# Kernel tuning notes

Hardware: AMD Instinct MI355X
Metric: run time of the kernel (lower is better)

The kernel has to match this reference:

```python
import jax, jax.numpy as jnp
import numpy as np

N_WAY = 64

def setup_inputs() -> dict:
    key = jax.random.key(0)
    k1, k2, k3, k4 = jax.random.split(key, 4)
    S, Q, F, D = 1024, 16384, 2048, 512
    xs = jax.random.normal(k1, (S, F), dtype=jnp.float32)
    ys = jax.random.randint(k2, (S,), 0, N_WAY, dtype=jnp.int64)
    xq = jax.random.normal(k3, (Q, F), dtype=jnp.float32)
    W = jax.random.normal(k4, (F, D), dtype=jnp.float32) * 0.02
    b = jnp.zeros((D,), dtype=jnp.float32)
    return {"xs": xs, "ys": ys, "xq": xq, "W": W, "b": b}

def reference(xs, ys, xq, W, b):
    # encoder: linear projection [*, F] -> [*, D]
    z_s = xs @ W + b            # [S, D]
    z_q = xq @ W + b            # [Q, D]
    # class prototypes: segment mean over support embeddings -> [N_way, D]
    counts = jax.ops.segment_sum(jnp.ones_like(ys, dtype=z_s.dtype), ys, num_segments=N_WAY)
    proto = jax.ops.segment_sum(z_s, ys, num_segments=N_WAY) / jnp.clip(counts, 1.0)[:, None]
    # pairwise squared euclidean distance (expand + pow + sum), [Q, N_way]
    diff = z_q[:, None, :] - proto[None, :, :]   # [Q, N_way, D]
    dists = jnp.sum(diff * diff, axis=-1)
    return -dists
```

## Files before the change

### kernel.cpp

```cpp
#include <hip/hip_runtime.h>


typedef __attribute__((ext_vector_type(8))) short short8;
typedef __attribute__((ext_vector_type(4))) float floatx4;

#define S_ROWS 1024
#define F_DIM  2048
#define D_DIM  512
#define NWAY   64
#define Q_ROWS 16384

static __device__ __forceinline__ unsigned short f2bf(float f) {
  unsigned int u = __float_as_uint(f);
  u += 0x7FFF + ((u >> 16) & 1);
  return (unsigned short)(u >> 16);
}
static __device__ __forceinline__ float bf2f(unsigned short s) {
  return __uint_as_float(((unsigned int)s) << 16);
}

static __device__ __forceinline__ void load_lds16(const unsigned short* g, unsigned short* l) {
  __builtin_amdgcn_global_load_lds((const __attribute__((address_space(1))) unsigned int*)g,
                                   (__attribute__((address_space(3))) unsigned int*)l,
                                   16, 0, 0);
}

__global__ __launch_bounds__(256) void k0_transpose(const float* __restrict__ W,
                                                    unsigned short* __restrict__ Wt,
                                                    float* __restrict__ outz,
                                                    float* __restrict__ proto_acc) {
  __shared__ unsigned short t[64][65];
  int bx = blockIdx.x;
  int f0 = (bx >> 3) << 6;
  int d0 = (bx & 7) << 6;
  for (int j = 0; j < 16; j++) {
    int lin = j * 256 + threadIdx.x;
    int fl = lin >> 6, dl = lin & 63;
    t[fl][dl] = f2bf(W[(size_t)(f0 + fl) * 512 + d0 + dl]);
  }
  __syncthreads();
  for (int j = 0; j < 16; j++) {
    int lin = j * 256 + threadIdx.x;
    int dl = lin >> 6, fl = lin & 63;
    Wt[(size_t)(d0 + dl) * 2048 + f0 + fl] = t[fl][dl];
  }
  int tid = threadIdx.x;
  float4 zz = {0.f, 0.f, 0.f, 0.f};
#pragma unroll
  for (int p = 0; p < 4; p++)
    *(float4*)&outz[(size_t)bx * 4096 + p * 1024 + tid * 4] = zz;
  if (tid < 128) proto_acc[bx * 128 + tid] = 0.f;
}

__global__ __launch_bounds__(256) void k0_sort(const int* __restrict__ ys,
                                               int* __restrict__ order,
                                               int* __restrict__ starts,
                                               float* __restrict__ counts) {
  __shared__ int cnt[NWAY];
  __shared__ int st[NWAY + 1];
  __shared__ int wp[NWAY];
  int tid = threadIdx.x;
  if (tid < NWAY) cnt[tid] = 0;
  __syncthreads();
  for (int j = tid; j < S_ROWS; j += 256) atomicAdd(&cnt[ys[j]], 1);
  __syncthreads();
  if (tid == 0) {
    int a = 0;
    for (int c = 0; c < NWAY; c++) { st[c] = a; wp[c] = a; a += cnt[c]; }
    st[NWAY] = a;
  }
  __syncthreads();
  for (int j = tid; j < S_ROWS; j += 256) {
    int c = ys[j];
    int p = atomicAdd(&wp[c], 1);
    order[p] = j;
  }
  if (tid < NWAY) counts[tid] = (float)cnt[tid];
  if (tid < NWAY + 1) starts[tid] = st[tid];
}

__global__ __launch_bounds__(256) void k1_csum(const float* __restrict__ xs,
                                               const int* __restrict__ order,
                                               const int* __restrict__ starts,
                                               float* __restrict__ csum) {
  __shared__ int lord[S_ROWS];
  int c = blockIdx.x >> 1;
  int tid = threadIdx.x;
  int s = starts[c], e = starts[c + 1];
  int len = e - s;
  for (int j = tid; j < len; j += 256) lord[j] = order[s + j];
  __syncthreads();
  int f0 = (blockIdx.x & 1) * 1024 + tid * 4;
  float4 a = {0.f, 0.f, 0.f, 0.f};
  for (int i = 0; i < len; i++) {
    float4 v = *(const float4*)&xs[(size_t)lord[i] * F_DIM + f0];
    a.x += v.x; a.y += v.y; a.z += v.z; a.w += v.w;
  }
  *(float4*)&csum[(size_t)c * F_DIM + f0] = a;
}

__global__ __launch_bounds__(256) void k2_proto(const float* __restrict__ W,
                                               const float* __restrict__ csum,
                                               float* __restrict__ proto_acc) {
  __shared__ float cs[256];
  int bx = blockIdx.x;
  int c = bx >> 4;
  int dh = ((bx >> 3) & 1) * 256;
  int fc = (bx & 7) * 256;
  int tid = threadIdx.x;
  cs[tid] = csum[(size_t)c * F_DIM + fc + tid];
  __syncthreads();
  float a0 = 0.f;
#pragma unroll 8
  for (int f = 0; f < 256; f++)
    a0 += cs[f] * W[(size_t)(fc + f) * 512 + dh + tid];
  atomicAdd(&proto_acc[c * 512 + dh + tid], a0);
}

__global__ __launch_bounds__(256) void k2b_finalize(const float* __restrict__ proto_acc,
                                                    const float* __restrict__ b,
                                                    const float* __restrict__ counts,
                                                    unsigned short* __restrict__ proto_bf,
                                                    float* __restrict__ pnorm_part) {
  __shared__ float red[256];
  int n = blockIdx.x, tid = threadIdx.x;
  float cntv = counts[n];
  float inv = 1.f / fmaxf(cntv, 1.f);
  float qsq[2];
#pragma unroll
  for (int h = 0; h < 2; h++) {
    int d = h * 256 + tid;
    float p = (proto_acc[n * 512 + d] + cntv * b[d]) * inv;
    unsigned short hh = f2bf(p);
    proto_bf[(size_t)n * 512 + d] = hh;
    float q = bf2f(hh);
    qsq[h] = q * q;
  }
#pragma unroll
  for (int h = 0; h < 2; h++) {
    __syncthreads();
    red[tid] = qsq[h];
    __syncthreads();
    for (int s = 64; s > 0; s >>= 1) {
      if ((tid & 127) < s) red[tid] += red[tid + s];
      __syncthreads();
    }
    if (tid == 0) pnorm_part[(h * 2 + 0) * 64 + n] = red[0];
    if (tid == 128) pnorm_part[(h * 2 + 1) * 64 + n] = red[128];
  }
}

__global__ __launch_bounds__(256) void k_cvt(const float* __restrict__ xq,
                                             unsigned short* __restrict__ xqb) {
  size_t i = ((size_t)blockIdx.x * 256 + threadIdx.x) * 8;
  float4 v0 = *(const float4*)&xq[i];
  float4 v1 = *(const float4*)&xq[i + 4];
  ushort4 w0, w1;
  w0.x = f2bf(v0.x); w0.y = f2bf(v0.y); w0.z = f2bf(v0.z); w0.w = f2bf(v0.w);
  w1.x = f2bf(v1.x); w1.y = f2bf(v1.y); w1.z = f2bf(v1.z); w1.w = f2bf(v1.w);
  *(ushort4*)&xqb[i] = w0;
  *(ushort4*)&xqb[i + 4] = w1;
}

#define ZS_LD 136
__global__ __launch_bounds__(256) void k3_fused(const unsigned short* __restrict__ xqb,
                                                const unsigned short* __restrict__ Wt,
                                                const float* __restrict__ b,
                                                const unsigned short* __restrict__ proto_bf,
                                                const float* __restrict__ pnorm_part,
                                                float* __restrict__ out) {
  __shared__ __align__(16) char smem[53248];
  unsigned short* lA = (unsigned short*)smem;
  unsigned short* lB = (unsigned short*)(smem + 8192);
  unsigned short* zs = (unsigned short*)smem;
  unsigned short* pb = (unsigned short*)(smem + 34816);
  float* qnf = (float*)(smem + 52224);
  float* pnl = (float*)(smem + 52736);

  int tid = threadIdx.x;
  int bx = blockIdx.x;
  int xcd = bx & 7;
  int g = bx >> 3;
  int m0 = (xcd * 16 + (g & 15)) * 128;
  int n0 = (g >> 4) * 128;
  int slice = g >> 4;

  int wave = tid >> 6, lane = tid & 63;
  int wm = (wave & 1) * 64, wn = (wave >> 1) * 64;
  int lrow = lane & 15, lquad = lane >> 4;

  floatx4 acc[4][4];
#pragma unroll
  for (int i = 0; i < 4; i++)
#pragma unroll
    for (int j = 0; j < 4; j++) acc[i][j] = (floatx4){0.f, 0.f, 0.f, 0.f};

  int c0 = wave * 64 + lane;

  for (int k0 = 0; k0 < F_DIM; k0 += 32) {
#pragma unroll
    for (int i = 0; i < 2; i++) {
      int c = i * 256 + c0;
      int row = c >> 2, k8 = (c & 3) * 8;
      load_lds16(&xqb[(size_t)(m0 + row) * F_DIM + k0 + k8],
                 &lA[(size_t)(i * 256 + wave * 64) * 8]);
      load_lds16(&Wt[(size_t)(n0 + row) * F_DIM + k0 + k8],
                 &lB[(size_t)(i * 256 + wave * 64) * 8]);
    }
    __syncthreads();
    short8 af[4], bfr[4];
#pragma unroll
    for (int i = 0; i < 4; i++) af[i] = *(const short8*)&lA[(wm + i * 16 + lrow) * 32 + lquad * 8];
#pragma unroll
    for (int j = 0; j < 4; j++) bfr[j] = *(const short8*)&lB[(wn + j * 16 + lrow) * 32 + lquad * 8];
#pragma unroll
    for (int i = 0; i < 4; i++)
#pragma unroll
      for (int j = 0; j < 4; j++)
        acc[i][j] = __builtin_amdgcn_mfma_f32_16x16x32_bf16(af[i], bfr[j], acc[i][j], 0, 0, 0);
    __syncthreads();
  }

  if (tid < 128) qnf[tid] = 0.f;
  if (tid < 64) pnl[tid] = pnorm_part[slice * 64 + tid];
  __syncthreads();

#pragma unroll
  for (int i = 0; i < 4; i++) {
    float rn[4] = {0.f, 0.f, 0.f, 0.f};
#pragma unroll
    for (int j = 0; j < 4; j++) {
      int ld = wn + j * 16 + lrow;
      float bb = b[n0 + ld];
#pragma unroll
      for (int r = 0; r < 4; r++) {
        int rl = wm + i * 16 + lquad * 4 + r;
        float v = acc[i][j][r] + bb;
        unsigned short h = f2bf(v);
        zs[rl * ZS_LD + ld] = h;
        float vq = bf2f(h);
        rn[r] += vq * vq;
      }
    }
#pragma unroll
    for (int r = 0; r < 4; r++) {
      float s = rn[r];
      s += __shfl_xor(s, 1, 16);
      s += __shfl_xor(s, 2, 16);
      s += __shfl_xor(s, 4, 16);
      s += __shfl_xor(s, 8, 16);
      if (lrow == 0) atomicAdd(&qnf[wm + i * 16 + lquad * 4 + r], s);
    }
  }

#pragma unroll
  for (int p = 0; p < 4; p++) {
    int ch = p * 256 + tid;
    int row = ch >> 4, l8 = (ch & 15) * 8;
    *(short8*)&pb[row * ZS_LD + l8] =
        *(const short8*)&proto_bf[(size_t)row * 512 + n0 + l8];
  }
  __syncthreads();

  floatx4 acc2[2][4];
#pragma unroll
  for (int i = 0; i < 2; i++)
#pragma unroll
    for (int j = 0; j < 4; j++) acc2[i][j] = (floatx4){0.f, 0.f, 0.f, 0.f};

#pragma unroll
  for (int ks = 0; ks < 4; ks++) {
    short8 af2[2], bf2[4];
#pragma unroll
    for (int i = 0; i < 2; i++)
      af2[i] = *(const short8*)&zs[(wave * 32 + i * 16 + lrow) * ZS_LD + ks * 32 + lquad * 8];
#pragma unroll
    for (int j = 0; j < 4; j++)
      bf2[j] = *(const short8*)&pb[(j * 16 + lrow) * ZS_LD + ks * 32 + lquad * 8];
#pragma unroll
    for (int i = 0; i < 2; i++)
#pragma unroll
      for (int j = 0; j < 4; j++)
        acc2[i][j] = __builtin_amdgcn_mfma_f32_16x16x32_bf16(af2[i], bf2[j], acc2[i][j], 0, 0, 0);
  }

#pragma unroll
  for (int i = 0; i < 2; i++) {
#pragma unroll
    for (int j = 0; j < 4; j++) {
      int c = j * 16 + lrow;
      float pn = pnl[c];
#pragma unroll
      for (int r = 0; r < 4; r++) {
        int ql = wave * 32 + i * 16 + lquad * 4 + r;
        float val = 2.f * acc2[i][j][r] - qnf[ql] - pn;
        atomicAdd(&out[(size_t)(m0 + ql) * 64 + c], val);
      }
    }
  }
}

extern "C" void kernel_launch(void* const* d_in, const int* in_sizes, int n_in,
                              void* d_out, int out_size, void* d_ws, size_t ws_size,
                              hipStream_t stream) {
  const float* xs = (const float*)d_in[0];
  const int* ys = (const int*)d_in[1];
  const float* xq = (const float*)d_in[2];
  const float* W = (const float*)d_in[3];
  const float* b = (const float*)d_in[4];
  float* out = (float*)d_out;
  char* ws = (char*)d_ws;

  size_t off = 0;
  auto take = [&](size_t bytes) -> char* {
    char* r = ws + off;
    off += (bytes + 255) & ~(size_t)255;
    return r;
  };
  unsigned short* Wt = (unsigned short*)take((size_t)D_DIM * F_DIM * 2);
  float* csum = (float*)take((size_t)NWAY * F_DIM * 4);
  float* proto_acc = (float*)take((size_t)NWAY * D_DIM * 4);
  unsigned short* proto_bf = (unsigned short*)take((size_t)NWAY * D_DIM * 2);
  float* counts = (float*)take(NWAY * 4);
  float* pnorm_part = (float*)take(4 * NWAY * 4);
  int* order = (int*)take(S_ROWS * 4);
  int* starts = (int*)take((NWAY + 1) * 4);
  unsigned short* xqb = (unsigned short*)take((size_t)Q_ROWS * F_DIM * 2);

  k0_transpose<<<256, 256, 0, stream>>>(W, Wt, out, proto_acc);
  k0_sort<<<1, 256, 0, stream>>>(ys, order, starts, counts);
  k1_csum<<<128, 256, 0, stream>>>(xs, order, starts, csum);
  k2_proto<<<1024, 256, 0, stream>>>(W, csum, proto_acc);
  k2b_finalize<<<64, 256, 0, stream>>>(proto_acc, b, counts, proto_bf, pnorm_part);
  k_cvt<<<(Q_ROWS * F_DIM) / (256 * 8), 256, 0, stream>>>(xq, xqb);
  k3_fused<<<512, 256, 0, stream>>>(xqb, Wt, b, proto_bf, pnorm_part, out);
}
```

Baseline: 299.8 us.

## Fuse xq bf16 conversion into GEMM A-tile load and merge prep kernels

Removes the separate fp32-to-bf16 conversion pass over xq. The main GEMM kernel now loads fp32 rows directly, packs them to bf16 with a cheap round-half-up perm, and writes them to LDS, saving a full write and reread of a 64MB buffer. The transpose and label-sort kernels are merged into one launch with an extra block. In exchange, A loads become synchronous register loads instead of async global-to-LDS, and each of the 4 N-slices rereads fp32 xq, which doubles A traffic per slice and may expose latency in the unpipelined K loop.

```diff
diff --git a/kernel.cpp b/kernel.cpp
--- a/kernel.cpp
+++ b/kernel.cpp
@@ -18,6 +18,11 @@
 static __device__ __forceinline__ float bf2f(unsigned short s) {
   return __uint_as_float(((unsigned int)s) << 16);
 }
+static __device__ __forceinline__ unsigned int pack_bf2(float x, float y) {
+  unsigned int ux = __float_as_uint(x) + 0x8000u;
+  unsigned int uy = __float_as_uint(y) + 0x8000u;
+  return __builtin_amdgcn_perm(uy, ux, 0x07060302u);
+}
 
 static __device__ __forceinline__ void load_lds16(const unsigned short* g, unsigned short* l) {
   __builtin_amdgcn_global_load_lds((const __attribute__((address_space(1))) unsigned int*)g,
@@ -25,58 +30,58 @@
                                    16, 0, 0);
 }
 
-__global__ __launch_bounds__(256) void k0_transpose(const float* __restrict__ W,
-                                                    unsigned short* __restrict__ Wt,
-                                                    float* __restrict__ outz,
-                                                    float* __restrict__ proto_acc) {
+__global__ __launch_bounds__(256) void k_prep(const float* __restrict__ W,
+                                              unsigned short* __restrict__ Wt,
+                                              float* __restrict__ outz,
+                                              float* __restrict__ proto_acc,
+                                              const int* __restrict__ ys,
+                                              int* __restrict__ order,
+                                              int* __restrict__ starts,
+                                              float* __restrict__ counts) {
   __shared__ unsigned short t[64][65];
-  int bx = blockIdx.x;
-  int f0 = (bx >> 3) << 6;
-  int d0 = (bx & 7) << 6;
-  for (int j = 0; j < 16; j++) {
-    int lin = j * 256 + threadIdx.x;
-    int fl = lin >> 6, dl = lin & 63;
-    t[fl][dl] = f2bf(W[(size_t)(f0 + fl) * 512 + d0 + dl]);
-  }
-  __syncthreads();
-  for (int j = 0; j < 16; j++) {
-    int lin = j * 256 + threadIdx.x;
-    int dl = lin >> 6, fl = lin & 63;
-    Wt[(size_t)(d0 + dl) * 2048 + f0 + fl] = t[fl][dl];
-  }
-  int tid = threadIdx.x;
-  float4 zz = {0.f, 0.f, 0.f, 0.f};
-#pragma unroll
-  for (int p = 0; p < 4; p++)
-    *(float4*)&outz[(size_t)bx * 4096 + p * 1024 + tid * 4] = zz;
-  if (tid < 128) proto_acc[bx * 128 + tid] = 0.f;
-}
-
-__global__ __launch_bounds__(256) void k0_sort(const int* __restrict__ ys,
-                                               int* __restrict__ order,
-                                               int* __restrict__ starts,
-                                               float* __restrict__ counts) {
   __shared__ int cnt[NWAY];
   __shared__ int st[NWAY + 1];
   __shared__ int wp[NWAY];
+  int bx = blockIdx.x;
   int tid = threadIdx.x;
-  if (tid < NWAY) cnt[tid] = 0;
-  __syncthreads();
-  for (int j = tid; j < S_ROWS; j += 256) atomicAdd(&cnt[ys[j]], 1);
-  __syncthreads();
-  if (tid == 0) {
-    int a = 0;
-    for (int c = 0; c < NWAY; c++) { st[c] = a; wp[c] = a; a += cnt[c]; }
-    st[NWAY] = a;
-  }
-  __syncthreads();
-  for (int j = tid; j < S_ROWS; j += 256) {
-    int c = ys[j];
-    int p = atomicAdd(&wp[c], 1);
-    order[p] = j;
-  }
-  if (tid < NWAY) counts[tid] = (float)cnt[tid];
-  if (tid < NWAY + 1) starts[tid] = st[tid];
+  if (bx < 256) {
+    int f0 = (bx >> 3) << 6;
+    int d0 = (bx & 7) << 6;
+    for (int j = 0; j < 16; j++) {
+      int lin = j * 256 + tid;
+      int fl = lin >> 6, dl = lin & 63;
+      t[fl][dl] = f2bf(W[(size_t)(f0 + fl) * 512 + d0 + dl]);
+    }
+    __syncthreads();
+    for (int j = 0; j < 16; j++) {
+      int lin = j * 256 + tid;
+      int dl = lin >> 6, fl = lin & 63;
+      Wt[(size_t)(d0 + dl) * 2048 + f0 + fl] = t[fl][dl];
+    }
+    float4 zz = {0.f, 0.f, 0.f, 0.f};
+#pragma unroll
+    for (int p = 0; p < 4; p++)
+      *(float4*)&outz[(size_t)bx * 4096 + p * 1024 + tid * 4] = zz;
+    if (tid < 128) proto_acc[bx * 128 + tid] = 0.f;
+  } else {
+    if (tid < NWAY) cnt[tid] = 0;
+    __syncthreads();
+    for (int j = tid; j < S_ROWS; j += 256) atomicAdd(&cnt[ys[j]], 1);
+    __syncthreads();
+    if (tid == 0) {
+      int a = 0;
+      for (int c = 0; c < NWAY; c++) { st[c] = a; wp[c] = a; a += cnt[c]; }
+      st[NWAY] = a;
+    }
+    __syncthreads();
+    for (int j = tid; j < S_ROWS; j += 256) {
+      int c = ys[j];
+      int p = atomicAdd(&wp[c], 1);
+      order[p] = j;
+    }
+    if (tid < NWAY) counts[tid] = (float)cnt[tid];
+    if (tid < NWAY + 1) starts[tid] = st[tid];
+  }
 }
 
 __global__ __launch_bounds__(256) void k1_csum(const float* __restrict__ xs,
@@ -150,20 +155,8 @@
   }
 }
 
-__global__ __launch_bounds__(256) void k_cvt(const float* __restrict__ xq,
-                                             unsigned short* __restrict__ xqb) {
-  size_t i = ((size_t)blockIdx.x * 256 + threadIdx.x) * 8;
-  float4 v0 = *(const float4*)&xq[i];
-  float4 v1 = *(const float4*)&xq[i + 4];
-  ushort4 w0, w1;
-  w0.x = f2bf(v0.x); w0.y = f2bf(v0.y); w0.z = f2bf(v0.z); w0.w = f2bf(v0.w);
-  w1.x = f2bf(v1.x); w1.y = f2bf(v1.y); w1.z = f2bf(v1.z); w1.w = f2bf(v1.w);
-  *(ushort4*)&xqb[i] = w0;
-  *(ushort4*)&xqb[i + 4] = w1;
-}
-
 #define ZS_LD 136
-__global__ __launch_bounds__(256) void k3_fused(const unsigned short* __restrict__ xqb,
+__global__ __launch_bounds__(256) void k3_fused(const float* __restrict__ xq,
                                                 const unsigned short* __restrict__ Wt,
                                                 const float* __restrict__ b,
                                                 const unsigned short* __restrict__ proto_bf,
@@ -196,17 +189,29 @@
     for (int j = 0; j < 4; j++) acc[i][j] = (floatx4){0.f, 0.f, 0.f, 0.f};
 
   int c0 = wave * 64 + lane;
+  int arow = tid >> 1, akh = (tid & 1) * 16;
+  const float* agp = &xq[(size_t)(m0 + arow) * F_DIM + akh];
+  unsigned int* lAu = (unsigned int*)&lA[arow * 32 + akh];
 
   for (int k0 = 0; k0 < F_DIM; k0 += 32) {
+    float4 va0 = *(const float4*)(agp + k0);
+    float4 va1 = *(const float4*)(agp + k0 + 4);
+    float4 va2 = *(const float4*)(agp + k0 + 8);
+    float4 va3 = *(const float4*)(agp + k0 + 12);
 #pragma unroll
     for (int i = 0; i < 2; i++) {
       int c = i * 256 + c0;
       int row = c >> 2, k8 = (c & 3) * 8;
-      load_lds16(&xqb[(size_t)(m0 + row) * F_DIM + k0 + k8],
-                 &lA[(size_t)(i * 256 + wave * 64) * 8]);
       load_lds16(&Wt[(size_t)(n0 + row) * F_DIM + k0 + k8],
                  &lB[(size_t)(i * 256 + wave * 64) * 8]);
     }
+    uint4 w0, w1;
+    w0.x = pack_bf2(va0.x, va0.y); w0.y = pack_bf2(va0.z, va0.w);
+    w0.z = pack_bf2(va1.x, va1.y); w0.w = pack_bf2(va1.z, va1.w);
+    w1.x = pack_bf2(va2.x, va2.y); w1.y = pack_bf2(va2.z, va2.w);
+    w1.z = pack_bf2(va3.x, va3.y); w1.w = pack_bf2(va3.z, va3.w);
+    *(uint4*)lAu = w0;
+    *(uint4*)(lAu + 4) = w1;
     __syncthreads();
     short8 af[4], bfr[4];
 #pragma unroll
@@ -270,18 +275,18 @@
 
 #pragma unroll
   for (int ks = 0; ks < 4; ks++) {
-    short8 af2[2], bf2[4];
+    short8 af2[2], bf2r[4];
 #pragma unroll
     for (int i = 0; i < 2; i++)
       af2[i] = *(const short8*)&zs[(wave * 32 + i * 16 + lrow) * ZS_LD + ks * 32 + lquad * 8];
 #pragma unroll
     for (int j = 0; j < 4; j++)
-      bf2[j] = *(const short8*)&pb[(j * 16 + lrow) * ZS_LD + ks * 32 + lquad * 8];
+      bf2r[j] = *(const short8*)&pb[(j * 16 + lrow) * ZS_LD + ks * 32 + lquad * 8];
 #pragma unroll
     for (int i = 0; i < 2; i++)
 #pragma unroll
       for (int j = 0; j < 4; j++)
-        acc2[i][j] = __builtin_amdgcn_mfma_f32_16x16x32_bf16(af2[i], bf2[j], acc2[i][j], 0, 0, 0);
+        acc2[i][j] = __builtin_amdgcn_mfma_f32_16x16x32_bf16(af2[i], bf2r[j], acc2[i][j], 0, 0, 0);
   }
 
 #pragma unroll
@@ -325,13 +330,10 @@
   float* pnorm_part = (float*)take(4 * NWAY * 4);
   int* order = (int*)take(S_ROWS * 4);
   int* starts = (int*)take((NWAY + 1) * 4);
-  unsigned short* xqb = (unsigned short*)take((size_t)Q_ROWS * F_DIM * 2);
-
-  k0_transpose<<<256, 256, 0, stream>>>(W, Wt, out, proto_acc);
-  k0_sort<<<1, 256, 0, stream>>>(ys, order, starts, counts);
+
+  k_prep<<<257, 256, 0, stream>>>(W, Wt, out, proto_acc, ys, order, starts, counts);
   k1_csum<<<128, 256, 0, stream>>>(xs, order, starts, csum);
   k2_proto<<<1024, 256, 0, stream>>>(W, csum, proto_acc);
   k2b_finalize<<<64, 256, 0, stream>>>(proto_acc, b, counts, proto_bf, pnorm_part);
-  k_cvt<<<(Q_ROWS * F_DIM) / (256 * 8), 256, 0, stream>>>(xq, xqb);
-  k3_fused<<<512, 256, 0, stream>>>(xqb, Wt, b, proto_bf, pnorm_part, out);
-}
+  k3_fused<<<512, 256, 0, stream>>>(xq, Wt, b, proto_bf, pnorm_part, out);
+}
```

After: 291.6 us. 2.7% less time.
